# Optimization experiments

Measured on AMD Instinct MI355X. Metric: run time of the kernel, lower is better.

The kernel has to match this reference:

```python
import jax, jax.numpy as jnp
import numpy as np
from jax import lax

EPS = 1e-5

def _layernorm_c(x, w, b):
    # WithBias LayerNorm over channel dim (to_3d puts C last; equivalent to axis=1 here)
    mu = x.mean(axis=1, keepdims=True)
    var = x.var(axis=1, keepdims=True)
    return (x - mu) / jnp.sqrt(var + EPS) * w[None, :, None, None] + b[None, :, None, None]

def _conv1x1(x, W, b=None):
    y = jnp.einsum('bchw,oc->bohw', x, W)
    if b is not None:
        y = y + b[None, :, None, None]
    return y

def _dwconv3x3(x, k):
    # k: [C, 1, 3, 3], groups = C
    return lax.conv_general_dilated(
        x, k, window_strides=(1, 1), padding='SAME',
        dimension_numbers=('NCHW', 'OIHW', 'NCHW'),
        feature_group_count=k.shape[0])

def setup_inputs() -> dict:
    key = jax.random.key(0)
    B, C, H, W = 4, 128, 96, 256
    ks = jax.random.split(key, 12)
    s = 0.05
    return {
        'x_l': jax.random.normal(ks[0], (B, C, H, W), jnp.float32),
        'x_r': jax.random.normal(ks[1], (B, C, H, W), jnp.float32),
        'Wl_m': jax.random.normal(ks[2], (2 * C, C), jnp.float32) * s,
        'Wr_m': jax.random.normal(ks[3], (2 * C, C), jnp.float32) * s,
        'dw_l': jax.random.normal(ks[4], (2 * C, 1, 3, 3), jnp.float32) * s,
        'dw_r': jax.random.normal(ks[5], (2 * C, 1, 3, 3), jnp.float32) * s,
        'lnl_w': jnp.ones((C,), jnp.float32),
        'lnl_b': jnp.zeros((C,), jnp.float32),
        'lnr_w': jnp.ones((C,), jnp.float32),
        'lnr_b': jnp.zeros((C,), jnp.float32),
        'Wq_l': jax.random.normal(ks[6], (C, C), jnp.float32) * s,
        'bq_l': jnp.zeros((C,), jnp.float32),
        'Wq_r': jax.random.normal(ks[7], (C, C), jnp.float32) * s,
        'bq_r': jnp.zeros((C,), jnp.float32),
        'beta': jax.random.normal(ks[8], (1, C, 1, 1), jnp.float32) * s,
        'gamma': jax.random.normal(ks[9], (1, C, 1, 1), jnp.float32) * s,
    }

def reference(x_l, x_r, Wl_m, Wr_m, dw_l, dw_r, lnl_w, lnl_b, lnr_w, lnr_b,
              Wq_l, bq_l, Wq_r, bq_r, beta, gamma):
    c = x_l.shape[1]
    scale = c ** -0.5
    fusion_l = _dwconv3x3(_conv1x1(x_l, Wl_m), dw_l)   # [b,2c,h,w]
    V_l, l_mid = jnp.split(fusion_l, 2, axis=1)
    fusion_r = _dwconv3x3(_conv1x1(x_r, Wr_m), dw_r)
    V_r, r_mid = jnp.split(fusion_r, 2, axis=1)
    Q_l = _conv1x1(_layernorm_c(l_mid, lnl_w, lnl_b), Wq_l, bq_l)  # [b,c,h,w]
    Q_r = _conv1x1(_layernorm_c(r_mid, lnr_w, lnr_b), Wq_r, bq_r)  # [b,c,h,w]
    # row-wise attention over width: [b,h,w,w]
    attn = jnp.einsum('bchw,bchv->bhwv', Q_l, Q_r) * scale
    # F_r2l: softmax over last axis (v), contract V_r over v
    F_r2l = jnp.einsum('bhwv,bchv->bchw', jax.nn.softmax(attn, axis=-1), V_r)
    # F_l2r: softmax of attn^T over its last axis == softmax over w (axis=-2)
    F_l2r = jnp.einsum('bhwv,bchw->bchv', jax.nn.softmax(attn, axis=-2), V_l)
    out_l = x_l + F_r2l * beta
    out_r = x_r + F_l2r * gamma
    return (out_l, out_r)
```

## Files before the change

### kernel.cpp

```cpp
#include <hip/hip_runtime.h>
#include <hip/hip_bf16.h>

using bf16 = __hip_bfloat16;
typedef __attribute__((ext_vector_type(8))) short bf16x8;
typedef __attribute__((ext_vector_type(2))) float f32x2;
typedef __attribute__((ext_vector_type(4))) float f32x4;
typedef __attribute__((ext_vector_type(16))) float f32x16;
typedef __attribute__((ext_vector_type(4))) unsigned int u32x4;

#define DEVI __device__ __forceinline__

constexpr int B = 4, C = 128, C2 = 256, H = 96, W = 256;
constexpr int HW = H * W;
constexpr int NPIX = B * HW;
constexpr int BH = B * H;
constexpr float SCALE = 0.08838834764831845f;
constexpr float LN_EPS = 1e-5f;

DEVI float lo16(unsigned u) { return __builtin_bit_cast(float, u << 16); }
DEVI float hi16(unsigned u) { return __builtin_bit_cast(float, u & 0xffff0000u); }
DEVI unsigned short f2bu(float v) {
    bf16 b = __float2bfloat16(v);
    return __builtin_bit_cast(unsigned short, b);
}
DEVI unsigned packbf2(float a, float b) {
    return (unsigned)f2bu(a) | ((unsigned)f2bu(b) << 16);
}
DEVI f32x2 up2(unsigned p) { return f32x2{lo16(p), hi16(p)}; }

__global__ __launch_bounds__(256) void wcvt_kernel(
    const float* __restrict__ w0, const float* __restrict__ w1,
    const float* __restrict__ w2, const float* __restrict__ w3,
    unsigned short* __restrict__ o0, unsigned short* __restrict__ o1,
    unsigned short* __restrict__ o2, unsigned short* __restrict__ o3)
{
    const int id = blockIdx.x, t = threadIdx.x;
    const float* src; unsigned short* dst; int base;
    if (id < 8)       { src = w0; dst = o0; base = id * 4096; }
    else if (id < 16) { src = w1; dst = o1; base = (id - 8) * 4096; }
    else if (id < 20) { src = w2; dst = o2; base = (id - 16) * 4096; }
    else              { src = w3; dst = o3; base = (id - 20) * 4096; }
#pragma unroll
    for (int u = 0; u < 4; ++u) {
        int i = base + t * 16 + u * 4;
        float4 v = *reinterpret_cast<const float4*>(&src[i]);
        ushort4 o;
        o.x = f2bu(v.x); o.y = f2bu(v.y); o.z = f2bu(v.z); o.w = f2bu(v.w);
        *reinterpret_cast<ushort4*>(&dst[i]) = o;
    }
}

__global__ __launch_bounds__(256) void conv1x1_mfma_kernel(
    const float* __restrict__ x_l, const float* __restrict__ x_r,
    const unsigned short* __restrict__ Wb_l, const unsigned short* __restrict__ Wb_r,
    unsigned short* __restrict__ y_l, unsigned short* __restrict__ y_r)
{
    __shared__ unsigned short xs[64][132];
    const int side = blockIdx.x & 1;
    const int u = blockIdx.x >> 1;
    const float* x = side ? x_r : x_l;
    const unsigned short* Wb = side ? Wb_r : Wb_l;
    unsigned short* y = side ? y_r : y_l;

    const int t = threadIdx.x;
    const int b = u / (HW / 64);
    const int hw0 = (u % (HW / 64)) * 64;

#pragma unroll
    for (int i = 0; i < 8; ++i) {
        const int idx = t + i * 256;
        const int px4 = (idx & 15) * 4;
        const int c = idx >> 4;
        float4 v = *reinterpret_cast<const float4*>(&x[((size_t)b * C + c) * HW + hw0 + px4]);
        xs[px4 + 0][c] = f2bu(v.x);
        xs[px4 + 1][c] = f2bu(v.y);
        xs[px4 + 2][c] = f2bu(v.z);
        xs[px4 + 3][c] = f2bu(v.w);
    }
    __syncthreads();

    const int lane = t & 63, wid = t >> 6;
    const int l15 = lane & 15, l4 = lane >> 4;

    f32x4 acc[4][4] = {};
    for (int kk = 0; kk < 4; ++kk) {
        const int k0 = kk * 32 + l4 * 8;
        bf16x8 a[4], bb[4];
#pragma unroll
        for (int mt = 0; mt < 4; ++mt)
            a[mt] = *reinterpret_cast<const bf16x8*>(&xs[mt * 16 + l15][k0]);
#pragma unroll
        for (int nt = 0; nt < 4; ++nt)
            bb[nt] = *reinterpret_cast<const bf16x8*>(
                &Wb[(size_t)(wid * 64 + nt * 16 + l15) * C + k0]);
#pragma unroll
        for (int mt = 0; mt < 4; ++mt)
#pragma unroll
            for (int nt = 0; nt < 4; ++nt)
                acc[mt][nt] = __builtin_amdgcn_mfma_f32_16x16x32_bf16(bb[nt], a[mt], acc[mt][nt], 0, 0, 0);
    }
#pragma unroll
    for (int mt = 0; mt < 4; ++mt) {
        const size_t px = (size_t)(b * HW + hw0 + mt * 16 + l15);
#pragma unroll
        for (int nt = 0; nt < 4; ++nt) {
            const int oc = wid * 64 + nt * 16 + l4 * 4;
            uint2 o;
            o.x = packbf2(acc[mt][nt][0], acc[mt][nt][1]);
            o.y = packbf2(acc[mt][nt][2], acc[mt][nt][3]);
            *reinterpret_cast<uint2*>(&y[px * C2 + oc]) = o;
        }
    }
}

__global__ __launch_bounds__(256, 3) void dwlnq_kernel(
    const unsigned short* __restrict__ y_l, const unsigned short* __restrict__ y_r,
    const float* __restrict__ dwk_l, const float* __restrict__ dwk_r,
    const float* __restrict__ lnw_l, const float* __restrict__ lnb_l,
    const float* __restrict__ lnw_r, const float* __restrict__ lnb_r,
    const unsigned short* __restrict__ Wq_l, const unsigned short* __restrict__ Wq_r,
    const float* __restrict__ bq_l, const float* __restrict__ bq_r,
    unsigned short* __restrict__ VT_l, unsigned short* __restrict__ VT_r,
    unsigned short* __restrict__ q_l, unsigned short* __restrict__ q_r)
{
    __shared__ unsigned short ts[64][128];
    __shared__ unsigned char msb[64 * 256];
    __shared__ float lnwb[256];

    const int side = blockIdx.x & 1;
    const int u = blockIdx.x >> 1;
    const unsigned short* y = side ? y_r : y_l;
    const float* dwk = side ? dwk_r : dwk_l;
    const float* lnw = side ? lnw_r : lnw_l;
    const float* lnb = side ? lnb_r : lnb_l;
    const unsigned short* Wqb = side ? Wq_r : Wq_l;
    const float* bq = side ? bq_r : bq_l;
    unsigned short* VT = side ? VT_r : VT_l;
    unsigned short* q = side ? q_r : q_l;

    const int t = threadIdx.x;
    const int wt = u & 3;
    const int bh = u >> 2;
    const int h = bh % H;
    const int ch8 = t & 31, wi = t >> 5;
    const int c0 = ch8 * 8;
    const int wbase = wt * 64 + wi * 8;

    lnwb[t] = (t < 128) ? lnw[t] : lnb[t - 128];

    f32x2 acc2[8][4] = {};
#pragma unroll
    for (int dh = 0; dh < 3; ++dh) {
        const int hh = h + dh - 1;
        if ((unsigned)hh >= (unsigned)H) continue;
        f32x2 wt0[4], wt1[4], wt2[4];
#pragma unroll
        for (int k = 0; k < 4; ++k) {
            const float* d0 = dwk + (c0 + 2 * k) * 9 + dh * 3;
            const float* d1 = dwk + (c0 + 2 * k + 1) * 9 + dh * 3;
            wt0[k] = f32x2{d0[0], d1[0]};
            wt1[k] = f32x2{d0[1], d1[1]};
            wt2[k] = f32x2{d0[2], d1[2]};
        }
        const unsigned short* yrow = y + (size_t)(bh + dh - 1) * W * C2 + c0;
        uint4 uu[10];
#pragma unroll
        for (int j = 0; j < 10; ++j) {
            const int ww = wbase - 1 + j;
            uint4 v = {0u, 0u, 0u, 0u};
            if ((unsigned)ww < 256u)
                v = *reinterpret_cast<const uint4*>(&yrow[(size_t)ww * C2]);
            uu[j] = v;
        }
#pragma unroll
        for (int j = 0; j < 10; ++j) {
            const unsigned arr[4] = {uu[j].x, uu[j].y, uu[j].z, uu[j].w};
            f32x2 v[4];
#pragma unroll
            for (int k = 0; k < 4; ++k) v[k] = up2(arr[k]);
            if (j < 8) {
#pragma unroll
                for (int k = 0; k < 4; ++k) acc2[j][k] += v[k] * wt0[k];
            }
            if (j >= 1 && j <= 8) {
#pragma unroll
                for (int k = 0; k < 4; ++k) acc2[j - 1][k] += v[k] * wt1[k];
            }
            if (j >= 2) {
#pragma unroll
                for (int k = 0; k < 4; ++k) acc2[j - 2][k] += v[k] * wt2[k];
            }
        }
    }

#pragma unroll
    for (int i = 0; i < 8; ++i) {
        uint4 o;
        o.x = packbf2(acc2[i][0].x, acc2[i][0].y);
        o.y = packbf2(acc2[i][1].x, acc2[i][1].y);
        o.z = packbf2(acc2[i][2].x, acc2[i][2].y);
        o.w = packbf2(acc2[i][3].x, acc2[i][3].y);
        const int pxl = wi * 8 + i;
        if (c0 < 128) {
            *reinterpret_cast<uint4*>(&ts[pxl][c0]) = o;
        } else {
            const unsigned addr =
                (unsigned)(pxl * 256 + (c0 - 128) * 2) ^ (unsigned)((pxl & 7) << 4);
            *reinterpret_cast<uint4*>(msb + addr) = o;
        }
    }
    __syncthreads();

#pragma unroll
    for (int it = 0; it < 4; ++it) {
        const int idx = t + it * 256;
        const int c = idx & 127, w8 = idx >> 7;
        unsigned short vals[8];
#pragma unroll
        for (int k = 0; k < 8; ++k) vals[k] = ts[w8 * 8 + k][c];
        unsigned short* dst = &VT[((size_t)bh * C + c) * W + wt * 64 + w8 * 8];
        *reinterpret_cast<ushort4*>(dst)     = *reinterpret_cast<const ushort4*>(&vals[0]);
        *reinterpret_cast<ushort4*>(dst + 4) = *reinterpret_cast<const ushort4*>(&vals[4]);
    }

    {
        const int px = t >> 2, qq = t & 3;
        uint4 raw[4];
#pragma unroll
        for (int v = 0; v < 4; ++v) {
            const unsigned addr =
                (unsigned)(px * 256 + qq * 64 + v * 16) ^ (unsigned)((px & 7) << 4);
            raw[v] = *reinterpret_cast<const uint4*>(msb + addr);
        }
        float s1 = 0.f, s2 = 0.f;
#pragma unroll
        for (int v = 0; v < 4; ++v) {
            const unsigned arr[4] = {raw[v].x, raw[v].y, raw[v].z, raw[v].w};
#pragma unroll
            for (int k = 0; k < 4; ++k) {
                float v0 = lo16(arr[k]), v1 = hi16(arr[k]);
                s1 += v0 + v1; s2 += v0 * v0 + v1 * v1;
            }
        }
        s1 += __shfl_xor(s1, 1); s2 += __shfl_xor(s2, 1);
        s1 += __shfl_xor(s1, 2); s2 += __shfl_xor(s2, 2);
        const float mu = s1 * (1.f / C);
        const float rs = rsqrtf(s2 * (1.f / C) - mu * mu + LN_EPS);
#pragma unroll
        for (int v = 0; v < 4; ++v) {
            const unsigned arr[4] = {raw[v].x, raw[v].y, raw[v].z, raw[v].w};
            float nv[8];
#pragma unroll
            for (int k = 0; k < 4; ++k) {
                int c = qq * 32 + v * 8 + k * 2;
                nv[k * 2]     = (lo16(arr[k]) - mu) * rs * lnwb[c] + lnwb[128 + c];
                nv[k * 2 + 1] = (hi16(arr[k]) - mu) * rs * lnwb[c + 1] + lnwb[128 + c + 1];
            }
            uint4 wv;
            wv.x = packbf2(nv[0], nv[1]); wv.y = packbf2(nv[2], nv[3]);
            wv.z = packbf2(nv[4], nv[5]); wv.w = packbf2(nv[6], nv[7]);
            const unsigned addr =
                (unsigned)(px * 256 + qq * 64 + v * 16) ^ (unsigned)((px & 7) << 4);
            *reinterpret_cast<uint4*>(msb + addr) = wv;
        }
    }
    __syncthreads();

    {
        const int lane = t & 63, wid = t >> 6;
        const int l15 = lane & 15, l4 = lane >> 4;
        f32x4 acc[8] = {};
        for (int kk = 0; kk < 4; ++kk) {
            const int k0 = kk * 32 + l4 * 8;
            const int pxl = wid * 16 + l15;
            const unsigned aaddr =
                (unsigned)(pxl * 256 + k0 * 2) ^ (unsigned)((pxl & 7) << 4);
            bf16x8 a = *reinterpret_cast<const bf16x8*>(msb + aaddr);
#pragma unroll
            for (int nt = 0; nt < 8; ++nt) {
                bf16x8 bv = *reinterpret_cast<const bf16x8*>(
                    &Wqb[(size_t)(nt * 16 + l15) * C + k0]);
                acc[nt] = __builtin_amdgcn_mfma_f32_16x16x32_bf16(a, bv, acc[nt], 0, 0, 0);
            }
        }
        const size_t px0 = (size_t)bh * W + wt * 64;
#pragma unroll
        for (int nt = 0; nt < 8; ++nt) {
            const int oc = nt * 16 + l15;
            const float bias = bq[oc];
#pragma unroll
            for (int r = 0; r < 4; ++r) {
                const int pxr = wid * 16 + l4 * 4 + r;
                q[(px0 + pxr) * C + oc] = f2bu(acc[nt][r] + bias);
            }
        }
    }
}

__global__ __launch_bounds__(256, 2) void fused_attn_kernel(
    const unsigned short* __restrict__ Q_l, const unsigned short* __restrict__ Q_r,
    const unsigned short* __restrict__ VT_l, const unsigned short* __restrict__ VT_r,
    const float* __restrict__ x_l, const float* __restrict__ x_r,
    const float* __restrict__ beta, const float* __restrict__ gamma,
    float* __restrict__ out_l, float* __restrict__ out_r)
{
    __shared__ __align__(16) unsigned char lds[65536];
    const int bid = blockIdx.x;
    const int xcd = bid & 7;
    const int local = bid >> 3;
    const int bh = xcd * 48 + (local >> 2);
    const int sub = local & 3;
    const int side = sub & 1, half = sub >> 1;

    const unsigned short* Q  = side ? Q_r : Q_l;
    const unsigned short* K  = side ? Q_l : Q_r;
    const unsigned short* VT = side ? VT_l : VT_r;
    const float* x    = side ? x_r : x_l;
    const float* coef = side ? gamma : beta;
    float* out        = side ? out_r : out_l;

    const int t = threadIdx.x;
    const int lane = t & 63, wv = t >> 6;
    const int l31 = lane & 31, hi = lane >> 5;
    const int b = bh / H, h = bh % H;
    const int w0 = half * 128 + wv * 32;

    const unsigned short* qrow = Q + ((size_t)bh * W + w0 + l31) * C + hi * 8;
    bf16x8 qfrag[8];
#pragma unroll
    for (int ks = 0; ks < 8; ++ks)
        qfrag[ks] = *reinterpret_cast<const bf16x8*>(qrow + ks * 16);

    const char* kg = (const char*)(K + (size_t)bh * W * C);
    const char* vg = (const char*)(VT + (size_t)bh * C * W);
    const int srow = lane >> 4;
    const int scol = (lane & 15) * 16;

    float sden_loc = 0.f;
    f32x16 oacc[4] = {};

    for (int ci = 0; ci < 2; ++ci) {
#pragma unroll
        for (int i = 0; i < 8; ++i) {
            const int r0 = wv * 32 + i * 4;
            const int row = r0 + srow;
            const char* src = kg + (size_t)(ci * 128 + row) * 256 + (scol ^ ((row & 7) << 4));
            __builtin_amdgcn_global_load_lds(
                (const __attribute__((address_space(1))) void*)src,
                (__attribute__((address_space(3))) void*)(lds + r0 * 256), 16, 0, 0);
        }
#pragma unroll
        for (int i = 0; i < 8; ++i) {
            const int r0 = wv * 32 + i * 4;
            const int row = r0 + srow;
            const char* src = vg + (size_t)row * 512 + ci * 256 + (scol ^ ((row & 7) << 4));
            __builtin_amdgcn_global_load_lds(
                (const __attribute__((address_space(1))) void*)src,
                (__attribute__((address_space(3))) void*)(lds + 32768 + r0 * 256), 16, 0, 0);
        }
        __syncthreads();

        f32x16 sacc[4] = {};
        __builtin_amdgcn_s_setprio(1);
#pragma unroll
        for (int vt = 0; vt < 4; ++vt) {
            const int row = vt * 32 + l31;
            const unsigned rb = row * 256;
            const unsigned sw = (row & 7) << 4;
#pragma unroll
            for (int ks = 0; ks < 8; ++ks) {
                bf16x8 a = *reinterpret_cast<const bf16x8*>(
                    lds + rb + ((ks * 32 + hi * 16) ^ sw));
                sacc[vt] = __builtin_amdgcn_mfma_f32_32x32x16_bf16(a, qfrag[ks], sacc[vt], 0, 0, 0);
            }
        }
        __builtin_amdgcn_s_setprio(0);

#pragma unroll
        for (int vt = 0; vt < 4; ++vt)
#pragma unroll
            for (int r = 0; r < 16; ++r) {
                float e = __expf(sacc[vt][r] * SCALE);
                sacc[vt][r] = e;
                sden_loc += e;
            }

        unsigned pw[8][4];
#pragma unroll
        for (int g = 0; g < 8; ++g) {
            const int vt = g >> 1, bs = (g & 1) * 8;
            unsigned pa = packbf2(sacc[vt][bs + 0], sacc[vt][bs + 1]);
            unsigned pc = packbf2(sacc[vt][bs + 2], sacc[vt][bs + 3]);
            unsigned pb = packbf2(sacc[vt][bs + 4], sacc[vt][bs + 5]);
            unsigned pd = packbf2(sacc[vt][bs + 6], sacc[vt][bs + 7]);
            unsigned sa = __shfl_xor(pa, 32);
            unsigned sb = __shfl_xor(pb, 32);
            unsigned sc = __shfl_xor(pc, 32);
            unsigned sd = __shfl_xor(pd, 32);
            pw[g][0] = hi ? sb : pa;
            pw[g][1] = hi ? sd : pc;
            pw[g][2] = hi ? pb : sa;
            pw[g][3] = hi ? pd : sc;
        }

        __builtin_amdgcn_s_setprio(1);
#pragma unroll
        for (int ct = 0; ct < 4; ++ct) {
            const int row = ct * 32 + l31;
            const unsigned rb = 32768 + row * 256;
            const unsigned sw = (row & 7) << 4;
#pragma unroll
            for (int g = 0; g < 8; ++g) {
                bf16x8 va = *reinterpret_cast<const bf16x8*>(
                    lds + rb + ((g * 32 + hi * 16) ^ sw));
                u32x4 pv = {pw[g][0], pw[g][1], pw[g][2], pw[g][3]};
                oacc[ct] = __builtin_amdgcn_mfma_f32_32x32x16_bf16(
                    va, __builtin_bit_cast(bf16x8, pv), oacc[ct], 0, 0, 0);
            }
        }
        __builtin_amdgcn_s_setprio(0);
        __syncthreads();
    }

    const float sden = sden_loc + __shfl_xor(sden_loc, 32);
    const float inv = 1.f / sden;
    const size_t base0 = (size_t)b * C * HW + (size_t)h * W + w0 + l31;
#pragma unroll
    for (int ct = 0; ct < 4; ++ct)
#pragma unroll
        for (int r = 0; r < 16; ++r) {
            const int c = ct * 32 + (r & 3) + 8 * (r >> 2) + 4 * hi;
            const size_t a = base0 + (size_t)c * HW;
            out[a] = x[a] + oacc[ct][r] * inv * coef[c];
        }
}

extern "C" void kernel_launch(void* const* d_in, const int* in_sizes, int n_in,
                              void* d_out, int out_size, void* d_ws, size_t ws_size,
                              hipStream_t stream) {
    (void)in_sizes; (void)n_in; (void)out_size; (void)ws_size;
    const float* x_l   = (const float*)d_in[0];
    const float* x_r   = (const float*)d_in[1];
    const float* Wl_m  = (const float*)d_in[2];
    const float* Wr_m  = (const float*)d_in[3];
    const float* dw_l  = (const float*)d_in[4];
    const float* dw_r  = (const float*)d_in[5];
    const float* lnl_w = (const float*)d_in[6];
    const float* lnl_b = (const float*)d_in[7];
    const float* lnr_w = (const float*)d_in[8];
    const float* lnr_b = (const float*)d_in[9];
    const float* Wq_l  = (const float*)d_in[10];
    const float* bq_l  = (const float*)d_in[11];
    const float* Wq_r  = (const float*)d_in[12];
    const float* bq_r  = (const float*)d_in[13];
    const float* beta  = (const float*)d_in[14];
    const float* gamma = (const float*)d_in[15];

    char* ws = (char*)d_ws;
    unsigned short* ymid_l   = (unsigned short*)(ws + 0);
    unsigned short* ymid_r   = (unsigned short*)(ws + 50331648);
    unsigned short* VT_l     = (unsigned short*)(ws + 150994944);
    unsigned short* VT_r     = (unsigned short*)(ws + 176160768);
    unsigned short* Q_l      = (unsigned short*)(ws + 201326592);
    unsigned short* Q_r      = (unsigned short*)(ws + 226492416);
    unsigned short* Wlb      = (unsigned short*)(ws + 251658240);
    unsigned short* Wrb      = (unsigned short*)(ws + 251723776);
    unsigned short* Wqlb     = (unsigned short*)(ws + 251789312);
    unsigned short* Wqrb     = (unsigned short*)(ws + 251822080);

    float* out_l = (float*)d_out;
    float* out_r = out_l + (size_t)B * C * HW;

    const dim3 blk(256);

    wcvt_kernel<<<24, blk, 0, stream>>>(Wl_m, Wr_m, Wq_l, Wq_r, Wlb, Wrb, Wqlb, Wqrb);

    conv1x1_mfma_kernel<<<3072, blk, 0, stream>>>(x_l, x_r, Wlb, Wrb, ymid_l, ymid_r);
    dwlnq_kernel<<<3072, blk, 0, stream>>>(ymid_l, ymid_r, dw_l, dw_r,
                                           lnl_w, lnl_b, lnr_w, lnr_b,
                                           Wqlb, Wqrb, bq_l, bq_r,
                                           VT_l, VT_r, Q_l, Q_r);
    fused_attn_kernel<<<1536, blk, 0, stream>>>(Q_l, Q_r, VT_l, VT_r,
                                                x_l, x_r, beta, gamma, out_l, out_r);
}
```

Measured before the change: 229.8 us.

## Split depthwise-conv/LN/Q kernel into separate V and mid-branch kernels

Measured after the change: 229.9 us. No clear change (+0.0%).

```diff
diff --git a/kernel.cpp b/kernel.cpp
--- a/kernel.cpp
+++ b/kernel.cpp
@@ -113,17 +113,89 @@
     }
 }
 
-__global__ __launch_bounds__(256, 3) void dwlnq_kernel(
+__global__ __launch_bounds__(128) void dwv_kernel(
+    const unsigned short* __restrict__ y_l, const unsigned short* __restrict__ y_r,
+    const float* __restrict__ dwk_l, const float* __restrict__ dwk_r,
+    unsigned short* __restrict__ VT_l, unsigned short* __restrict__ VT_r)
+{
+    const int side = blockIdx.x & 1;
+    const int u = blockIdx.x >> 1;
+    const unsigned short* y = side ? y_r : y_l;
+    const float* dwk = side ? dwk_r : dwk_l;
+    unsigned short* VT = side ? VT_r : VT_l;
+
+    const int t = threadIdx.x;
+    const int wt = u & 3;
+    const int bh = u >> 2;
+    const int h = bh % H;
+    const int ch8 = t & 15, wi = t >> 4;
+    const int c0 = ch8 * 8;
+    const int wbase = wt * 64 + wi * 8;
+
+    f32x2 acc2[8][4] = {};
+#pragma unroll
+    for (int dh = 0; dh < 3; ++dh) {
+        const int hh = h + dh - 1;
+        if ((unsigned)hh >= (unsigned)H) continue;
+        f32x2 wt0[4], wt1[4], wt2[4];
+#pragma unroll
+        for (int k = 0; k < 4; ++k) {
+            const float* d0 = dwk + (c0 + 2 * k) * 9 + dh * 3;
+            const float* d1 = dwk + (c0 + 2 * k + 1) * 9 + dh * 3;
+            wt0[k] = f32x2{d0[0], d1[0]};
+            wt1[k] = f32x2{d0[1], d1[1]};
+            wt2[k] = f32x2{d0[2], d1[2]};
+        }
+        const unsigned short* yrow = y + (size_t)(bh + dh - 1) * W * C2 + c0;
+        uint4 uu[10];
+#pragma unroll
+        for (int j = 0; j < 10; ++j) {
+            const int ww = wbase - 1 + j;
+            uint4 v = {0u, 0u, 0u, 0u};
+            if ((unsigned)ww < 256u)
+                v = *reinterpret_cast<const uint4*>(&yrow[(size_t)ww * C2]);
+            uu[j] = v;
+        }
+#pragma unroll
+        for (int j = 0; j < 10; ++j) {
+            const unsigned arr[4] = {uu[j].x, uu[j].y, uu[j].z, uu[j].w};
+            f32x2 v[4];
+#pragma unroll
+            for (int k = 0; k < 4; ++k) v[k] = up2(arr[k]);
+            if (j < 8) {
+#pragma unroll
+                for (int k = 0; k < 4; ++k) acc2[j][k] += v[k] * wt0[k];
+            }
+            if (j >= 1 && j <= 8) {
+#pragma unroll
+                for (int k = 0; k < 4; ++k) acc2[j - 1][k] += v[k] * wt1[k];
+            }
+            if (j >= 2) {
+#pragma unroll
+                for (int k = 0; k < 4; ++k) acc2[j - 2][k] += v[k] * wt2[k];
+            }
+        }
+    }
+#pragma unroll
+    for (int k = 0; k < 8; ++k) {
+        uint4 o;
+        o.x = packbf2(acc2[0][k >> 1][k & 1], acc2[1][k >> 1][k & 1]);
+        o.y = packbf2(acc2[2][k >> 1][k & 1], acc2[3][k >> 1][k & 1]);
+        o.z = packbf2(acc2[4][k >> 1][k & 1], acc2[5][k >> 1][k & 1]);
+        o.w = packbf2(acc2[6][k >> 1][k & 1], acc2[7][k >> 1][k & 1]);
+        *reinterpret_cast<uint4*>(&VT[((size_t)bh * C + c0 + k) * W + wbase]) = o;
+    }
+}
+
+__global__ __launch_bounds__(128) void dwmid_kernel(
     const unsigned short* __restrict__ y_l, const unsigned short* __restrict__ y_r,
     const float* __restrict__ dwk_l, const float* __restrict__ dwk_r,
     const float* __restrict__ lnw_l, const float* __restrict__ lnb_l,
     const float* __restrict__ lnw_r, const float* __restrict__ lnb_r,
     const unsigned short* __restrict__ Wq_l, const unsigned short* __restrict__ Wq_r,
     const float* __restrict__ bq_l, const float* __restrict__ bq_r,
-    unsigned short* __restrict__ VT_l, unsigned short* __restrict__ VT_r,
     unsigned short* __restrict__ q_l, unsigned short* __restrict__ q_r)
 {
-    __shared__ unsigned short ts[64][128];
     __shared__ unsigned char msb[64 * 256];
     __shared__ float lnwb[256];
 
@@ -135,18 +207,18 @@
     const float* lnb = side ? lnb_r : lnb_l;
     const unsigned short* Wqb = side ? Wq_r : Wq_l;
     const float* bq = side ? bq_r : bq_l;
-    unsigned short* VT = side ? VT_r : VT_l;
     unsigned short* q = side ? q_r : q_l;
 
     const int t = threadIdx.x;
     const int wt = u & 3;
     const int bh = u >> 2;
     const int h = bh % H;
-    const int ch8 = t & 31, wi = t >> 5;
-    const int c0 = ch8 * 8;
+    const int ch8 = t & 15, wi = t >> 4;
+    const int c0m = ch8 * 8;
     const int wbase = wt * 64 + wi * 8;
 
-    lnwb[t] = (t < 128) ? lnw[t] : lnb[t - 128];
+    lnwb[t] = lnw[t];
+    lnwb[t + 128] = lnb[t];
 
     f32x2 acc2[8][4] = {};
 #pragma unroll
@@ -156,13 +228,13 @@
         f32x2 wt0[4], wt1[4], wt2[4];
 #pragma unroll
         for (int k = 0; k < 4; ++k) {
-            const float* d0 = dwk + (c0 + 2 * k) * 9 + dh * 3;
-            const float* d1 = dwk + (c0 + 2 * k + 1) * 9 + dh * 3;
+            const float* d0 = dwk + (128 + c0m + 2 * k) * 9 + dh * 3;
+            const float* d1 = dwk + (128 + c0m + 2 * k + 1) * 9 + dh * 3;
             wt0[k] = f32x2{d0[0], d1[0]};
             wt1[k] = f32x2{d0[1], d1[1]};
             wt2[k] = f32x2{d0[2], d1[2]};
         }
-        const unsigned short* yrow = y + (size_t)(bh + dh - 1) * W * C2 + c0;
+        const unsigned short* yrow = y + (size_t)(bh + dh - 1) * W * C2 + 128 + c0m;
         uint4 uu[10];
 #pragma unroll
         for (int j = 0; j < 10; ++j) {
@@ -201,40 +273,24 @@
         o.z = packbf2(acc2[i][2].x, acc2[i][2].y);
         o.w = packbf2(acc2[i][3].x, acc2[i][3].y);
         const int pxl = wi * 8 + i;
-        if (c0 < 128) {
-            *reinterpret_cast<uint4*>(&ts[pxl][c0]) = o;
-        } else {
+        const unsigned addr =
+            (unsigned)(pxl * 256 + c0m * 2) ^ (unsigned)((pxl & 7) << 4);
+        *reinterpret_cast<uint4*>(msb + addr) = o;
+    }
+    __syncthreads();
+
+    {
+        const int px = t >> 1, qq = t & 1;
+        uint4 raw[8];
+#pragma unroll
+        for (int v = 0; v < 8; ++v) {
             const unsigned addr =
-                (unsigned)(pxl * 256 + (c0 - 128) * 2) ^ (unsigned)((pxl & 7) << 4);
-            *reinterpret_cast<uint4*>(msb + addr) = o;
-        }
-    }
-    __syncthreads();
-
-#pragma unroll
-    for (int it = 0; it < 4; ++it) {
-        const int idx = t + it * 256;
-        const int c = idx & 127, w8 = idx >> 7;
-        unsigned short vals[8];
-#pragma unroll
-        for (int k = 0; k < 8; ++k) vals[k] = ts[w8 * 8 + k][c];
-        unsigned short* dst = &VT[((size_t)bh * C + c) * W + wt * 64 + w8 * 8];
-        *reinterpret_cast<ushort4*>(dst)     = *reinterpret_cast<const ushort4*>(&vals[0]);
-        *reinterpret_cast<ushort4*>(dst + 4) = *reinterpret_cast<const ushort4*>(&vals[4]);
-    }
-
-    {
-        const int px = t >> 2, qq = t & 3;
-        uint4 raw[4];
-#pragma unroll
-        for (int v = 0; v < 4; ++v) {
-            const unsigned addr =
-                (unsigned)(px * 256 + qq * 64 + v * 16) ^ (unsigned)((px & 7) << 4);
+                (unsigned)(px * 256 + qq * 128 + v * 16) ^ (unsigned)((px & 7) << 4);
             raw[v] = *reinterpret_cast<const uint4*>(msb + addr);
         }
         float s1 = 0.f, s2 = 0.f;
 #pragma unroll
-        for (int v = 0; v < 4; ++v) {
+        for (int v = 0; v < 8; ++v) {
             const unsigned arr[4] = {raw[v].x, raw[v].y, raw[v].z, raw[v].w};
 #pragma unroll
             for (int k = 0; k < 4; ++k) {
@@ -243,16 +299,15 @@
             }
         }
         s1 += __shfl_xor(s1, 1); s2 += __shfl_xor(s2, 1);
-        s1 += __shfl_xor(s1, 2); s2 += __shfl_xor(s2, 2);
         const float mu = s1 * (1.f / C);
         const float rs = rsqrtf(s2 * (1.f / C) - mu * mu + LN_EPS);
 #pragma unroll
-        for (int v = 0; v < 4; ++v) {
+        for (int v = 0; v < 8; ++v) {
             const unsigned arr[4] = {raw[v].x, raw[v].y, raw[v].z, raw[v].w};
             float nv[8];
 #pragma unroll
             for (int k = 0; k < 4; ++k) {
-                int c = qq * 32 + v * 8 + k * 2;
+                int c = qq * 64 + v * 8 + k * 2;
                 nv[k * 2]     = (lo16(arr[k]) - mu) * rs * lnwb[c] + lnwb[128 + c];
                 nv[k * 2 + 1] = (hi16(arr[k]) - mu) * rs * lnwb[c + 1] + lnwb[128 + c + 1];
             }
@@ -260,7 +315,7 @@
             wv.x = packbf2(nv[0], nv[1]); wv.y = packbf2(nv[2], nv[3]);
             wv.z = packbf2(nv[4], nv[5]); wv.w = packbf2(nv[6], nv[7]);
             const unsigned addr =
-                (unsigned)(px * 256 + qq * 64 + v * 16) ^ (unsigned)((px & 7) << 4);
+                (unsigned)(px * 256 + qq * 128 + v * 16) ^ (unsigned)((px & 7) << 4);
             *reinterpret_cast<uint4*>(msb + addr) = wv;
         }
     }
@@ -269,29 +324,38 @@
     {
         const int lane = t & 63, wid = t >> 6;
         const int l15 = lane & 15, l4 = lane >> 4;
-        f32x4 acc[8] = {};
+        f32x4 acc[2][8] = {};
         for (int kk = 0; kk < 4; ++kk) {
             const int k0 = kk * 32 + l4 * 8;
-            const int pxl = wid * 16 + l15;
-            const unsigned aaddr =
-                (unsigned)(pxl * 256 + k0 * 2) ^ (unsigned)((pxl & 7) << 4);
-            bf16x8 a = *reinterpret_cast<const bf16x8*>(msb + aaddr);
+            bf16x8 a[2];
+#pragma unroll
+            for (int pt = 0; pt < 2; ++pt) {
+                const int pxl = (wid * 2 + pt) * 16 + l15;
+                const unsigned aaddr =
+                    (unsigned)(pxl * 256 + k0 * 2) ^ (unsigned)((pxl & 7) << 4);
+                a[pt] = *reinterpret_cast<const bf16x8*>(msb + aaddr);
+            }
 #pragma unroll
             for (int nt = 0; nt < 8; ++nt) {
                 bf16x8 bv = *reinterpret_cast<const bf16x8*>(
                     &Wqb[(size_t)(nt * 16 + l15) * C + k0]);
-                acc[nt] = __builtin_amdgcn_mfma_f32_16x16x32_bf16(a, bv, acc[nt], 0, 0, 0);
+#pragma unroll
+                for (int pt = 0; pt < 2; ++pt)
+                    acc[pt][nt] = __builtin_amdgcn_mfma_f32_16x16x32_bf16(bv, a[pt], acc[pt][nt], 0, 0, 0);
             }
         }
         const size_t px0 = (size_t)bh * W + wt * 64;
 #pragma unroll
-        for (int nt = 0; nt < 8; ++nt) {
-            const int oc = nt * 16 + l15;
-            const float bias = bq[oc];
-#pragma unroll
-            for (int r = 0; r < 4; ++r) {
-                const int pxr = wid * 16 + l4 * 4 + r;
-                q[(px0 + pxr) * C + oc] = f2bu(acc[nt][r] + bias);
+        for (int pt = 0; pt < 2; ++pt) {
+            const size_t px = px0 + (wid * 2 + pt) * 16 + l15;
+#pragma unroll
+            for (int nt = 0; nt < 8; ++nt) {
+                const int oc = nt * 16 + l4 * 4;
+                const float4 bias = *reinterpret_cast<const float4*>(&bq[oc]);
+                uint2 o;
+                o.x = packbf2(acc[pt][nt][0] + bias.x, acc[pt][nt][1] + bias.y);
+                o.y = packbf2(acc[pt][nt][2] + bias.z, acc[pt][nt][3] + bias.w);
+                *reinterpret_cast<uint2*>(&q[px * C + oc]) = o;
             }
         }
     }
@@ -476,10 +540,10 @@
     wcvt_kernel<<<24, blk, 0, stream>>>(Wl_m, Wr_m, Wq_l, Wq_r, Wlb, Wrb, Wqlb, Wqrb);
 
     conv1x1_mfma_kernel<<<3072, blk, 0, stream>>>(x_l, x_r, Wlb, Wrb, ymid_l, ymid_r);
-    dwlnq_kernel<<<3072, blk, 0, stream>>>(ymid_l, ymid_r, dw_l, dw_r,
-                                           lnl_w, lnl_b, lnr_w, lnr_b,
-                                           Wqlb, Wqrb, bq_l, bq_r,
-                                           VT_l, VT_r, Q_l, Q_r);
+    dwv_kernel<<<3072, dim3(128), 0, stream>>>(ymid_l, ymid_r, dw_l, dw_r, VT_l, VT_r);
+    dwmid_kernel<<<3072, dim3(128), 0, stream>>>(ymid_l, ymid_r, dw_l, dw_r,
+                                                 lnl_w, lnl_b, lnr_w, lnr_b,
+                                                 Wqlb, Wqrb, bq_l, bq_r, Q_l, Q_r);
     fused_attn_kernel<<<1536, blk, 0, stream>>>(Q_l, Q_r, VT_l, VT_r,
                                                 x_l, x_r, beta, gamma, out_l, out_r);
 }
```
